# Kernel optimization log

Hardware: AMD Instinct MI355X
Metric: run time of the kernel (lower is better)

Reference implementation:

```python
import jax, jax.numpy as jnp
import numpy as np

B, T, H, L, FUT = 64, 256, 512, 4, 64


def setup_inputs() -> dict:
    key = jax.random.key(0)
    ks = jax.random.split(key, 8)
    s = 1.0 / np.sqrt(H)  # PyTorch LSTMCell/Linear default uniform init bound
    u = lambda k, shape: jax.random.uniform(k, shape, jnp.float32, -s, s)
    return {
        "iput": jax.random.normal(ks[0], (B, T), jnp.float32),
        "W_ih0": u(ks[1], (4 * H, 1)),        # layer 0 input->gates
        "W_ih": u(ks[2], (L - 1, 4 * H, H)),  # layers 1..L-1 input->gates
        "W_hh": u(ks[3], (L, 4 * H, H)),      # hidden->gates, all layers
        "b_ih": u(ks[4], (L, 4 * H)),
        "b_hh": u(ks[5], (L, 4 * H)),
        "W_lin": u(ks[6], (1, H)),            # readout Linear(H, 1)
        "b_lin": u(ks[7], (1,)),
        "future": FUT,
    }


def _cell(x, h, c, Wi, Wh, bi, bh):
    # PyTorch LSTMCell: gates ordered i, f, g, o
    g = x @ Wi.T + h @ Wh.T + bi + bh  # [B, 4H]
    i, f, gg, o = jnp.split(g, 4, axis=-1)
    c2 = jax.nn.sigmoid(f) * c + jax.nn.sigmoid(i) * jnp.tanh(gg)
    h2 = jax.nn.sigmoid(o) * jnp.tanh(c2)
    return h2, c2


def reference(iput, W_ih0, W_ih, W_hh, b_ih, b_hh, W_lin, b_lin, future):
    Lc = W_hh.shape[0]
    Bsz = iput.shape[0]
    Hd = W_hh.shape[-1]

    def layers(x, hs, cs):  # x: [B,1]; hs,cs: [L,B,H]
        for j in range(Lc):
            Wi = W_ih0 if j == 0 else W_ih[j - 1]
            inp = x if j == 0 else hs[j - 1]
            h2, c2 = _cell(inp, hs[j], cs[j], Wi, W_hh[j], b_ih[j], b_hh[j])
            hs = hs.at[j].set(h2)
            cs = cs.at[j].set(c2)
        return hs, cs

    hs0 = jnp.zeros((Lc, Bsz, Hd), iput.dtype)
    cs0 = jnp.zeros_like(hs0)

    def step_in(carry, x_t):  # x_t: [B]
        hs, cs = carry
        hs, cs = layers(x_t[:, None], hs, cs)
        out = hs[-1] @ W_lin.T + b_lin  # [B,1]
        return (hs, cs), out[:, 0]

    (hs, cs), outs = jax.lax.scan(step_in, (hs0, cs0), iput.T)  # outs: [T,B]

    def step_fut(carry, _):
        hs, cs, out = carry
        hs, cs = layers(out, hs, cs)
        out2 = hs[-1] @ W_lin.T + b_lin
        return (hs, cs, out2), out2[:, 0]

    last_out = outs[-1][:, None]  # feed last prediction back
    _, fouts = jax.lax.scan(step_fut, (hs, cs, last_out), None, length=future)

    return jnp.concatenate([outs, fouts], axis=0).T  # [B, T+future]
```

## Files before the change

### kernel.cpp

```cpp
#include <hip/hip_runtime.h>

#define Bsz 64
#define Tn 256
#define Hn 512
#define Ln 4
#define Gn 2048
#define TTn 320
#define NBLK 256
#define NTHR 512
#define HB (Hn * Bsz)
#define LHB (Ln * HB)
#define NPH_W (Tn + Ln - 1)

typedef float f32x4 __attribute__((ext_vector_type(4)));

#define OFF_WHH  0
#define OFF_WIH  (OFF_WHH + Ln * 8 * Hn)
#define OFF_PART (OFF_WIH + (Ln - 1) * 8 * Hn)
#define OFF_BS   (OFF_PART + 8 * 8 * Bsz)
#define OFF_W0   (OFF_BS + Ln * 8)
#define OFF_WLIN (OFF_W0 + 8)
#define OFF_RP   (OFF_WLIN + Hn)
#define OFF_XS   (OFF_RP + 8 * Bsz)
#define OFF_C    (OFF_XS + Bsz)
#define SMEM_FLOATS (OFF_C + Ln * 2 * Bsz)
#define SMEM_BYTES (SMEM_FLOATS * 4)

#define WS_BCOUNT   0
#define WS_ARRIVE   16
#define WS_MASTER   (16 + 16 * 32)
#define WS_BOOT     (WS_MASTER + 32)
#define WS_BOOTFLAG (WS_BOOT + 32)
#define WS_U32S     (WS_BOOTFLAG + 32)

__device__ float g_h[2 * LHB];
__device__ float g_hist[Tn * HB];
__device__ float g_p[Bsz * NBLK];
__device__ float g_xsg[Bsz];

__device__ __forceinline__ float sigm(float x) { return 1.0f / (1.0f + expf(-x)); }

__device__ __forceinline__ void fma4v(f32x4& a, const f32x4 h, const float w) {
    a.x = fmaf(h.x, w, a.x); a.y = fmaf(h.y, w, a.y);
    a.z = fmaf(h.z, w, a.z); a.w = fmaf(h.w, w, a.w);
}

#define GSTF(ptr, val) \
    asm volatile("global_store_dword %0, %1, off sc0 sc1" \
                 :: "v"(ptr), "v"(val) : "memory")
#define VMWAIT() asm volatile("s_waitcnt vmcnt(0)" ::: "memory")
#define L1INV() asm volatile("buffer_inv" ::: "memory")

__device__ __forceinline__ uint32_t rmw_add(uint32_t* p, uint32_t v) {
    return __hip_atomic_fetch_add(p, v, __ATOMIC_RELAXED, __HIP_MEMORY_SCOPE_AGENT);
}
__device__ __forceinline__ uint32_t ald(const uint32_t* p) {
    return __hip_atomic_load(p, __ATOMIC_RELAXED, __HIP_MEMORY_SCOPE_AGENT);
}
__device__ __forceinline__ uint32_t xcc_id() {
    uint32_t x;
    asm("s_getreg_b32 %0, hwreg(HW_REG_XCC_ID)" : "=s"(x));
    return x & 15u;
}

__device__ __forceinline__ void boot_bar(uint32_t* wsb, int tid) {
    VMWAIT();
    __syncthreads();
    if (tid == 0) {
        __builtin_amdgcn_fence(__ATOMIC_RELEASE, "agent");
        uint32_t old = rmw_add(wsb + WS_BOOT, 1u);
        if (old == NBLK - 1u) rmw_add(wsb + WS_BOOTFLAG, 1u);
        while (ald(wsb + WS_BOOTFLAG) < 1u) __builtin_amdgcn_s_sleep(2);
        __builtin_amdgcn_fence(__ATOMIC_ACQUIRE, "agent");
    }
    __syncthreads();
    asm volatile("" ::: "memory");
}

__device__ __forceinline__ void gbar(uint32_t* wsb, int tid, uint32_t x,
                                     uint32_t cnt_x, uint32_t& e) {
    ++e;
    VMWAIT();
    __syncthreads();
    if (tid == 0) {
        const uint32_t tgt = e * (uint32_t)NBLK;
        uint32_t old = rmw_add(wsb + WS_ARRIVE + x * 32, 1u);
        if (old == e * cnt_x - 1u) {
            __builtin_amdgcn_fence(__ATOMIC_ACQUIRE, "agent");
            VMWAIT();
            rmw_add(wsb + WS_MASTER, cnt_x);
            while (ald(wsb + WS_MASTER) < tgt) {}
        } else {
            while (ald(wsb + WS_MASTER) < tgt) {}
            L1INV();
            VMWAIT();
        }
    }
    __syncthreads();
    asm volatile("" ::: "memory");
}

__device__ __forceinline__ void gemm16(const float* __restrict__ w,
                                       const float* __restrict__ hbase,
                                       int k0, int b4, f32x4* acc) {
#pragma unroll
    for (int c = 0; c < 4; ++c) {
        const int k = k0 + c * 4;
        const float* hp = hbase + (size_t)k * Bsz + b4;
        const f32x4 h0 = *(const f32x4*)(hp);
        const f32x4 h1 = *(const f32x4*)(hp + Bsz);
        const f32x4 h2 = *(const f32x4*)(hp + 2 * Bsz);
        const f32x4 h3 = *(const f32x4*)(hp + 3 * Bsz);
#pragma unroll
        for (int r = 0; r < 8; ++r) {
            const f32x4 wv = *(const f32x4*)(w + r * Hn + k);
            fma4v(acc[r], h0, wv.x); fma4v(acc[r], h1, wv.y);
            fma4v(acc[r], h2, wv.z); fma4v(acc[r], h3, wv.w);
        }
    }
}

__global__ __launch_bounds__(NTHR, 1)
void lstm_seq(const float* __restrict__ iput,
              const float* __restrict__ Wih0,
              const float* __restrict__ Wih,
              const float* __restrict__ Whh,
              const float* __restrict__ bih,
              const float* __restrict__ bhh,
              const float* __restrict__ Wlin,
              const float* __restrict__ blin,
              float* __restrict__ out,
              uint32_t* __restrict__ wsb)
{
    extern __shared__ float sm[];
    const int bi  = blockIdx.x;
    const int tid = threadIdx.x;
    uint32_t e = 0;

    const uint32_t x = xcc_id();
    uint32_t cnt_x = 0;
    if (tid == 0) rmw_add(wsb + WS_BCOUNT + x, 1u);

    for (int i = tid; i < Ln * 8 * Hn; i += NTHR) {
        const int lyr = i >> 12, rem = i & 4095, r = rem >> 9, k = rem & 511;
        sm[OFF_WHH + i] = Whh[((size_t)(lyr * Gn + (r & 3) * Hn + bi * 2 + (r >> 2))) * Hn + k];
    }
    for (int i = tid; i < (Ln - 1) * 8 * Hn; i += NTHR) {
        const int lyr = i >> 12, rem = i & 4095, r = rem >> 9, k = rem & 511;
        sm[OFF_WIH + i] = Wih[((size_t)(lyr * Gn + (r & 3) * Hn + bi * 2 + (r >> 2))) * Hn + k];
    }
    if (tid < Ln * 8) {
        const int lyr = tid >> 3, r = tid & 7;
        const int gg = lyr * Gn + (r & 3) * Hn + bi * 2 + (r >> 2);
        sm[OFF_BS + tid] = bih[gg] + bhh[gg];
    }
    if (tid < 8) sm[OFF_W0 + tid] = Wih0[(tid & 3) * Hn + bi * 2 + (tid >> 2)];
    for (int i = tid; i < Hn; i += NTHR) sm[OFF_WLIN + i] = Wlin[i];
    for (int i = tid; i < Ln * 2 * Bsz; i += NTHR) sm[OFF_C + i] = 0.0f;

    for (int i = bi * NTHR + tid; i < 2 * LHB; i += NBLK * NTHR)
        GSTF(&g_h[i], 0.0f);

    const float blin0 = blin[0];
    boot_bar(wsb, tid);
    if (tid == 0) cnt_x = ald(wsb + WS_BCOUNT + x);

    {
        const int l   = tid >> 7;
        const int sub = tid & 127;
        const int bgw = sub & 15, b4w = bgw * 4;
        const int kgw = sub >> 4;
        const int k0w = kgw * 64;
        const int w2  = (tid >> 6) & 1;

        for (int s = 0; s < NPH_W; ++s) {
            const int pp = s & 1;
            float* cur        = g_h + pp * LHB;
            const float* prev = g_h + (pp ^ 1) * LHB;
            const int t = s - l;
            const bool act = ((unsigned)t < (unsigned)Tn);

            f32x4 acc[8];
#pragma unroll
            for (int r = 0; r < 8; ++r) acc[r] = (f32x4){0.f, 0.f, 0.f, 0.f};

            if (act) {
                {
                    const float* wh  = sm + OFF_WHH + l * 8 * Hn;
                    const float* hp0 = prev + (size_t)l * HB;
#pragma unroll 4
                    for (int c = 0; c < 16; ++c) {
                        const int k = k0w + (((c + (kgw & 3) * 4) & 15) << 2);
                        const float* hp = hp0 + (size_t)k * Bsz + b4w;
                        const f32x4 h0 = *(const f32x4*)(hp);
                        const f32x4 h1 = *(const f32x4*)(hp + Bsz);
                        const f32x4 h2 = *(const f32x4*)(hp + 2 * Bsz);
                        const f32x4 h3 = *(const f32x4*)(hp + 3 * Bsz);
#pragma unroll
                        for (int r = 0; r < 8; ++r) {
                            const f32x4 wv = *(const f32x4*)(wh + r * Hn + k);
                            fma4v(acc[r], h0, wv.x); fma4v(acc[r], h1, wv.y);
                            fma4v(acc[r], h2, wv.z); fma4v(acc[r], h3, wv.w);
                        }
                    }
                }
                if (l > 0) {
                    const float* wh  = sm + OFF_WIH + (l - 1) * 8 * Hn;
                    const float* hp0 = prev + (size_t)(l - 1) * HB;
#pragma unroll 4
                    for (int c = 0; c < 16; ++c) {
                        const int k = k0w + (((c + (kgw & 3) * 4) & 15) << 2);
                        const float* hp = hp0 + (size_t)k * Bsz + b4w;
                        const f32x4 h0 = *(const f32x4*)(hp);
                        const f32x4 h1 = *(const f32x4*)(hp + Bsz);
                        const f32x4 h2 = *(const f32x4*)(hp + 2 * Bsz);
                        const f32x4 h3 = *(const f32x4*)(hp + 3 * Bsz);
#pragma unroll
                        for (int r = 0; r < 8; ++r) {
                            const f32x4 wv = *(const f32x4*)(wh + r * Hn + k);
                            fma4v(acc[r], h0, wv.x); fma4v(acc[r], h1, wv.y);
                            fma4v(acc[r], h2, wv.z); fma4v(acc[r], h3, wv.w);
                        }
                    }
                }
            }

#pragma unroll
            for (int r = 0; r < 8; ++r) {
                f32x4 a = acc[r];
                a.x += __shfl_xor(a.x, 16); a.y += __shfl_xor(a.y, 16);
                a.z += __shfl_xor(a.z, 16); a.w += __shfl_xor(a.w, 16);
                a.x += __shfl_xor(a.x, 32); a.y += __shfl_xor(a.y, 32);
                a.z += __shfl_xor(a.z, 32); a.w += __shfl_xor(a.w, 32);
                acc[r] = a;
            }
            if ((tid & 48) == 0) {
#pragma unroll
                for (int r = 0; r < 8; ++r)
                    *(f32x4*)&sm[OFF_PART + ((l * 2 + w2) * 8 + r) * Bsz + b4w] = acc[r];
            }
            __syncthreads();

            {
                const int lb = tid >> 7, jl = (tid >> 6) & 1, b = tid & 63;
                const int tb = s - lb;
                if ((unsigned)tb < (unsigned)Tn) {
                    const int jg = bi * 2 + jl;
                    float gv[4];
#pragma unroll
                    for (int q = 0; q < 4; ++q) {
                        const int r = (jl << 2) | q;
                        gv[q] = sm[OFF_BS + lb * 8 + r]
                              + sm[OFF_PART + ((lb * 2 + 0) * 8 + r) * Bsz + b]
                              + sm[OFF_PART + ((lb * 2 + 1) * 8 + r) * Bsz + b];
                    }
                    if (lb == 0) {
                        const float xv = iput[b * Tn + s];
#pragma unroll
                        for (int q = 0; q < 4; ++q)
                            gv[q] = fmaf(xv, sm[OFF_W0 + ((jl << 2) | q)], gv[q]);
                    }
                    const float i_ = sigm(gv[0]);
                    const float f_ = sigm(gv[1]);
                    const float g_ = tanhf(gv[2]);
                    const float o_ = sigm(gv[3]);
                    float* cp = sm + OFF_C + (lb * 2 + jl) * Bsz + b;
                    const float c2 = fmaf(f_, *cp, i_ * g_);
                    *cp = c2;
                    const float h2 = o_ * tanhf(c2);
                    GSTF(&cur[((size_t)lb * Hn + jg) * Bsz + b], h2);
                    if (lb == 3)
                        GSTF(&g_hist[((size_t)tb * Hn + jg) * Bsz + b], h2);
                }
            }
            gbar(wsb, tid, x, cnt_x, e);
        }
    }

    {
        const int b = tid & 63, jq = tid >> 6;
        const float* hp = g_hist + ((size_t)bi * Hn + jq * 64) * Bsz + b;
        const float* wp = sm + OFF_WLIN + jq * 64;
        float r = 0.0f;
#pragma unroll 8
        for (int j = 0; j < 64; ++j) r = fmaf(hp[j * Bsz], wp[j], r);
        sm[OFF_RP + jq * Bsz + b] = r;
        if (tid < 256) {
            const int li = (tid >> 7) * 2 + 1;
            const int jl = (tid >> 6) & 1, bb = tid & 63;
            const size_t o = ((size_t)li * Hn + bi * 2 + jl) * Bsz + bb;
            const float v = g_h[o];
            GSTF(&g_h[LHB + o], v);
        }
        __syncthreads();
        if (tid < Bsz) {
            float xx = blin0;
#pragma unroll
            for (int q = 0; q < 8; ++q) xx += sm[OFF_RP + q * Bsz + tid];
            out[tid * TTn + bi] = xx;
            if (bi == 255) GSTF(&g_xsg[tid], xx);
        }
        gbar(wsb, tid, x, cnt_x, e);
    }

    {
        const int bg  = tid & 15, b4 = bg * 4;
        const int kg  = tid >> 4;
        const int k0  = kg * 16;
        const int wv_ = tid >> 6;

        for (int t = Tn; t < TTn; ++t) {
            const int ci = t & 1;
            float* hcur        = g_h + ci * LHB;
            const float* hprev = g_h + (ci ^ 1) * LHB;

            for (int lyr = 0; lyr < Ln; ++lyr) {
                if (lyr == 0 && tid < Bsz) {
                    float xx;
                    if (t == Tn) {
                        xx = g_xsg[tid];
                    } else {
                        const f32x4* pp2 = (const f32x4*)(g_p + tid * NBLK);
                        f32x4 s4 = {0.f, 0.f, 0.f, 0.f};
#pragma unroll 16
                        for (int q = 0; q < NBLK / 4; ++q) s4 += pp2[q];
                        xx = s4.x + s4.y + s4.z + s4.w + blin0;
                        if (bi == ((t - 1) & 255))
                            out[tid * TTn + (t - 1)] = xx;
                    }
                    sm[OFF_XS + tid] = xx;
                }

                f32x4 acc[8];
#pragma unroll
                for (int r = 0; r < 8; ++r) acc[r] = (f32x4){0.f, 0.f, 0.f, 0.f};

                if (lyr > 0)
                    gemm16(sm + OFF_WIH + (lyr - 1) * 8 * Hn,
                           hcur + (size_t)(lyr - 1) * HB, k0, b4, acc);
                gemm16(sm + OFF_WHH + lyr * 8 * Hn,
                       hprev + (size_t)lyr * HB, k0, b4, acc);

#pragma unroll
                for (int r = 0; r < 8; ++r) {
                    f32x4 a = acc[r];
                    a.x += __shfl_xor(a.x, 16); a.y += __shfl_xor(a.y, 16);
                    a.z += __shfl_xor(a.z, 16); a.w += __shfl_xor(a.w, 16);
                    a.x += __shfl_xor(a.x, 32); a.y += __shfl_xor(a.y, 32);
                    a.z += __shfl_xor(a.z, 32); a.w += __shfl_xor(a.w, 32);
                    acc[r] = a;
                }
                if ((tid & 48) == 0) {
#pragma unroll
                    for (int r = 0; r < 8; ++r)
                        *(f32x4*)&sm[OFF_PART + (wv_ * 8 + r) * Bsz + b4] = acc[r];
                }
                __syncthreads();

                float h2 = 0.0f;
                if (tid < 128) {
                    const int jl = tid >> 6, b = tid & 63;
                    const int jg = bi * 2 + jl;
                    float gv[4];
#pragma unroll
                    for (int q = 0; q < 4; ++q) {
                        const int r = (jl << 2) | q;
                        float v = sm[OFF_BS + lyr * 8 + r];
#pragma unroll
                        for (int p = 0; p < 8; ++p)
                            v += sm[OFF_PART + (p * 8 + r) * Bsz + b];
                        if (lyr == 0)
                            v = fmaf(sm[OFF_XS + b], sm[OFF_W0 + r], v);
                        gv[q] = v;
                    }
                    const float i_ = sigm(gv[0]);
                    const float f_ = sigm(gv[1]);
                    const float g_ = tanhf(gv[2]);
                    const float o_ = sigm(gv[3]);
                    float* cp = sm + OFF_C + (lyr * 2 + jl) * Bsz + b;
                    const float c2 = fmaf(f_, *cp, i_ * g_);
                    *cp = c2;
                    h2 = o_ * tanhf(c2);
                    GSTF(&hcur[((size_t)lyr * Hn + jg) * Bsz + b], h2);
                    if (lyr == 3 && jl == 1)
                        sm[OFF_RP + b] = h2 * sm[OFF_WLIN + jg];
                }
                if (lyr == 3) {
                    __syncthreads();
                    if (tid < Bsz) {
                        const float pv = fmaf(h2, sm[OFF_WLIN + bi * 2], sm[OFF_RP + tid]);
                        GSTF(&g_p[tid * NBLK + bi], pv);
                    }
                }

                gbar(wsb, tid, x, cnt_x, e);
            }
        }
    }

    if (bi == 0 && tid < Bsz) {
        const f32x4* pp2 = (const f32x4*)(g_p + tid * NBLK);
        f32x4 s4 = {0.f, 0.f, 0.f, 0.f};
#pragma unroll 16
        for (int q = 0; q < NBLK / 4; ++q) s4 += pp2[q];
        out[tid * TTn + (TTn - 1)] = s4.x + s4.y + s4.z + s4.w + blin0;
    }
}

extern "C" void kernel_launch(void* const* d_in, const int* in_sizes, int n_in,
                              void* d_out, int out_size, void* d_ws, size_t ws_size,
                              hipStream_t stream) {
    const float* iput = (const float*)d_in[0];
    const float* Wih0 = (const float*)d_in[1];
    const float* Wih  = (const float*)d_in[2];
    const float* Whh  = (const float*)d_in[3];
    const float* bih  = (const float*)d_in[4];
    const float* bhh  = (const float*)d_in[5];
    const float* Wlin = (const float*)d_in[6];
    const float* blin = (const float*)d_in[7];
    float* out = (float*)d_out;
    uint32_t* wsb = (uint32_t*)d_ws;

    (void)hipFuncSetAttribute((const void*)lstm_seq,
                              hipFuncAttributeMaxDynamicSharedMemorySize, SMEM_BYTES);

    (void)hipMemsetAsync(d_ws, 0, WS_U32S * sizeof(uint32_t), stream);

    void* args[] = {&iput, &Wih0, &Wih, &Whh, &bih, &bhh, &Wlin, &blin, &out, &wsb};
    hipLaunchCooperativeKernel((const void*)lstm_seq, dim3(NBLK), dim3(NTHR), args,
                               SMEM_BYTES, stream);
}
```

Measured before the change: 9.115 ms.

## Double threads per block and split gate GEMM rows across waves

Raises the block size from 512 to 1024 threads. Each wave now computes 2 gate rows over a quarter of K instead of 8 rows over a slice of K, which shrinks the per-thread accumulator set and the partial-sum reduction buffer. The wavefront pipeline, the readout partial sums and the autoregressive phase are all remapped to match. More resident waves could hide shared- and global-memory latency, but each wave now rereads the h vectors once per row pair rather than once per 8 rows, which raises total global/L2 load traffic.

```diff
diff --git a/kernel.cpp b/kernel.cpp
--- a/kernel.cpp
+++ b/kernel.cpp
@@ -7,7 +7,7 @@
 #define Gn 2048
 #define TTn 320
 #define NBLK 256
-#define NTHR 512
+#define NTHR 1024
 #define HB (Hn * Bsz)
 #define LHB (Ln * HB)
 #define NPH_W (Tn + Ln - 1)
@@ -17,11 +17,11 @@
 #define OFF_WHH  0
 #define OFF_WIH  (OFF_WHH + Ln * 8 * Hn)
 #define OFF_PART (OFF_WIH + (Ln - 1) * 8 * Hn)
-#define OFF_BS   (OFF_PART + 8 * 8 * Bsz)
+#define OFF_BS   (OFF_PART + 4 * 8 * Bsz)
 #define OFF_W0   (OFF_BS + Ln * 8)
 #define OFF_WLIN (OFF_W0 + 8)
 #define OFF_RP   (OFF_WLIN + Hn)
-#define OFF_XS   (OFF_RP + 8 * Bsz)
+#define OFF_XS   (OFF_RP + 16 * Bsz)
 #define OFF_C    (OFF_XS + Bsz)
 #define SMEM_FLOATS (OFF_C + Ln * 2 * Bsz)
 #define SMEM_BYTES (SMEM_FLOATS * 4)
@@ -100,24 +100,36 @@
     asm volatile("" ::: "memory");
 }
 
-__device__ __forceinline__ void gemm16(const float* __restrict__ w,
-                                       const float* __restrict__ hbase,
-                                       int k0, int b4, f32x4* acc) {
-#pragma unroll
-    for (int c = 0; c < 4; ++c) {
+template <int NITER>
+__device__ __forceinline__ void gemm_rows2(const float* __restrict__ wrow,
+                                           const float* __restrict__ hbase,
+                                           int k0, int b4, f32x4& a0, f32x4& a1) {
+#pragma unroll 4
+    for (int c = 0; c < NITER; ++c) {
         const int k = k0 + c * 4;
         const float* hp = hbase + (size_t)k * Bsz + b4;
         const f32x4 h0 = *(const f32x4*)(hp);
         const f32x4 h1 = *(const f32x4*)(hp + Bsz);
         const f32x4 h2 = *(const f32x4*)(hp + 2 * Bsz);
         const f32x4 h3 = *(const f32x4*)(hp + 3 * Bsz);
-#pragma unroll
-        for (int r = 0; r < 8; ++r) {
-            const f32x4 wv = *(const f32x4*)(w + r * Hn + k);
-            fma4v(acc[r], h0, wv.x); fma4v(acc[r], h1, wv.y);
-            fma4v(acc[r], h2, wv.z); fma4v(acc[r], h3, wv.w);
-        }
-    }
+        const f32x4 w0 = *(const f32x4*)(wrow + k);
+        const f32x4 w1 = *(const f32x4*)(wrow + Hn + k);
+        fma4v(a0, h0, w0.x); fma4v(a0, h1, w0.y);
+        fma4v(a0, h2, w0.z); fma4v(a0, h3, w0.w);
+        fma4v(a1, h0, w1.x); fma4v(a1, h1, w1.y);
+        fma4v(a1, h2, w1.z); fma4v(a1, h3, w1.w);
+    }
+}
+
+__device__ __forceinline__ void wave_reduce2(f32x4& a0, f32x4& a1) {
+    a0.x += __shfl_xor(a0.x, 16); a0.y += __shfl_xor(a0.y, 16);
+    a0.z += __shfl_xor(a0.z, 16); a0.w += __shfl_xor(a0.w, 16);
+    a1.x += __shfl_xor(a1.x, 16); a1.y += __shfl_xor(a1.y, 16);
+    a1.z += __shfl_xor(a1.z, 16); a1.w += __shfl_xor(a1.w, 16);
+    a0.x += __shfl_xor(a0.x, 32); a0.y += __shfl_xor(a0.y, 32);
+    a0.z += __shfl_xor(a0.z, 32); a0.w += __shfl_xor(a0.w, 32);
+    a1.x += __shfl_xor(a1.x, 32); a1.y += __shfl_xor(a1.y, 32);
+    a1.z += __shfl_xor(a1.z, 32); a1.w += __shfl_xor(a1.w, 32);
 }
 
 __global__ __launch_bounds__(NTHR, 1)
@@ -166,12 +178,13 @@
     if (tid == 0) cnt_x = ald(wsb + WS_BCOUNT + x);
 
     {
-        const int l   = tid >> 7;
-        const int sub = tid & 127;
+        const int l   = tid >> 8;
+        const int sub = tid & 255;
         const int bgw = sub & 15, b4w = bgw * 4;
-        const int kgw = sub >> 4;
-        const int k0w = kgw * 64;
-        const int w2  = (tid >> 6) & 1;
+        const int kq  = (sub >> 4) & 3;
+        const int w2  = sub >> 6;
+        const int k0w = kq * 128;
+        const int r0  = w2 * 2;
 
         for (int s = 0; s < NPH_W; ++s) {
             const int pp = s & 1;
@@ -180,68 +193,22 @@
             const int t = s - l;
             const bool act = ((unsigned)t < (unsigned)Tn);
 
-            f32x4 acc[8];
-#pragma unroll
-            for (int r = 0; r < 8; ++r) acc[r] = (f32x4){0.f, 0.f, 0.f, 0.f};
-
+            f32x4 a0 = {0.f, 0.f, 0.f, 0.f}, a1 = {0.f, 0.f, 0.f, 0.f};
             if (act) {
-                {
-                    const float* wh  = sm + OFF_WHH + l * 8 * Hn;
-                    const float* hp0 = prev + (size_t)l * HB;
-#pragma unroll 4
-                    for (int c = 0; c < 16; ++c) {
-                        const int k = k0w + (((c + (kgw & 3) * 4) & 15) << 2);
-                        const float* hp = hp0 + (size_t)k * Bsz + b4w;
-                        const f32x4 h0 = *(const f32x4*)(hp);
-                        const f32x4 h1 = *(const f32x4*)(hp + Bsz);
-                        const f32x4 h2 = *(const f32x4*)(hp + 2 * Bsz);
-                        const f32x4 h3 = *(const f32x4*)(hp + 3 * Bsz);
-#pragma unroll
-                        for (int r = 0; r < 8; ++r) {
-                            const f32x4 wv = *(const f32x4*)(wh + r * Hn + k);
-                            fma4v(acc[r], h0, wv.x); fma4v(acc[r], h1, wv.y);
-                            fma4v(acc[r], h2, wv.z); fma4v(acc[r], h3, wv.w);
-                        }
-                    }
-                }
-                if (l > 0) {
-                    const float* wh  = sm + OFF_WIH + (l - 1) * 8 * Hn;
-                    const float* hp0 = prev + (size_t)(l - 1) * HB;
-#pragma unroll 4
-                    for (int c = 0; c < 16; ++c) {
-                        const int k = k0w + (((c + (kgw & 3) * 4) & 15) << 2);
-                        const float* hp = hp0 + (size_t)k * Bsz + b4w;
-                        const f32x4 h0 = *(const f32x4*)(hp);
-                        const f32x4 h1 = *(const f32x4*)(hp + Bsz);
-                        const f32x4 h2 = *(const f32x4*)(hp + 2 * Bsz);
-                        const f32x4 h3 = *(const f32x4*)(hp + 3 * Bsz);
-#pragma unroll
-                        for (int r = 0; r < 8; ++r) {
-                            const f32x4 wv = *(const f32x4*)(wh + r * Hn + k);
-                            fma4v(acc[r], h0, wv.x); fma4v(acc[r], h1, wv.y);
-                            fma4v(acc[r], h2, wv.z); fma4v(acc[r], h3, wv.w);
-                        }
-                    }
-                }
+                gemm_rows2<32>(sm + OFF_WHH + (l * 8 + r0) * Hn,
+                               prev + (size_t)l * HB, k0w, b4w, a0, a1);
+                if (l > 0)
+                    gemm_rows2<32>(sm + OFF_WIH + ((l - 1) * 8 + r0) * Hn,
+                                   prev + (size_t)(l - 1) * HB, k0w, b4w, a0, a1);
             }
-
-#pragma unroll
-            for (int r = 0; r < 8; ++r) {
-                f32x4 a = acc[r];
-                a.x += __shfl_xor(a.x, 16); a.y += __shfl_xor(a.y, 16);
-                a.z += __shfl_xor(a.z, 16); a.w += __shfl_xor(a.w, 16);
-                a.x += __shfl_xor(a.x, 32); a.y += __shfl_xor(a.y, 32);
-                a.z += __shfl_xor(a.z, 32); a.w += __shfl_xor(a.w, 32);
-                acc[r] = a;
-            }
+            wave_reduce2(a0, a1);
             if ((tid & 48) == 0) {
-#pragma unroll
-                for (int r = 0; r < 8; ++r)
-                    *(f32x4*)&sm[OFF_PART + ((l * 2 + w2) * 8 + r) * Bsz + b4w] = acc[r];
+                *(f32x4*)&sm[OFF_PART + ((l * 8 + r0 + 0) * Bsz) + b4w] = a0;
+                *(f32x4*)&sm[OFF_PART + ((l * 8 + r0 + 1) * Bsz) + b4w] = a1;
             }
             __syncthreads();
 
-            {
+            if (tid < 512) {
                 const int lb = tid >> 7, jl = (tid >> 6) & 1, b = tid & 63;
                 const int tb = s - lb;
                 if ((unsigned)tb < (unsigned)Tn) {
@@ -251,8 +218,7 @@
                     for (int q = 0; q < 4; ++q) {
                         const int r = (jl << 2) | q;
                         gv[q] = sm[OFF_BS + lb * 8 + r]
-                              + sm[OFF_PART + ((lb * 2 + 0) * 8 + r) * Bsz + b]
-                              + sm[OFF_PART + ((lb * 2 + 1) * 8 + r) * Bsz + b];
+                              + sm[OFF_PART + (lb * 8 + r) * Bsz + b];
                     }
                     if (lb == 0) {
                         const float xv = iput[b * Tn + s];
@@ -279,11 +245,11 @@
 
     {
         const int b = tid & 63, jq = tid >> 6;
-        const float* hp = g_hist + ((size_t)bi * Hn + jq * 64) * Bsz + b;
-        const float* wp = sm + OFF_WLIN + jq * 64;
+        const float* hp = g_hist + ((size_t)bi * Hn + jq * 32) * Bsz + b;
+        const float* wp = sm + OFF_WLIN + jq * 32;
         float r = 0.0f;
 #pragma unroll 8
-        for (int j = 0; j < 64; ++j) r = fmaf(hp[j * Bsz], wp[j], r);
+        for (int j = 0; j < 32; ++j) r = fmaf(hp[j * Bsz], wp[j], r);
         sm[OFF_RP + jq * Bsz + b] = r;
         if (tid < 256) {
             const int li = (tid >> 7) * 2 + 1;
@@ -296,7 +262,7 @@
         if (tid < Bsz) {
             float xx = blin0;
 #pragma unroll
-            for (int q = 0; q < 8; ++q) xx += sm[OFF_RP + q * Bsz + tid];
+            for (int q = 0; q < 16; ++q) xx += sm[OFF_RP + q * Bsz + tid];
             out[tid * TTn + bi] = xx;
             if (bi == 255) GSTF(&g_xsg[tid], xx);
         }
@@ -305,9 +271,11 @@
 
     {
         const int bg  = tid & 15, b4 = bg * 4;
-        const int kg  = tid >> 4;
-        const int k0  = kg * 16;
-        const int wv_ = tid >> 6;
+        const int kq2 = (tid >> 4) & 3;
+        const int w   = tid >> 6;
+        const int r0  = (w & 3) * 2;
+        const int kh  = w >> 2;
+        const int k0  = kh * 128 + kq2 * 32;
 
         for (int t = Tn; t < TTn; ++t) {
             const int ci = t & 1;
@@ -331,29 +299,17 @@
                     sm[OFF_XS + tid] = xx;
                 }
 
-                f32x4 acc[8];
-#pragma unroll
-                for (int r = 0; r < 8; ++r) acc[r] = (f32x4){0.f, 0.f, 0.f, 0.f};
-
+                f32x4 a0 = {0.f, 0.f, 0.f, 0.f}, a1 = {0.f, 0.f, 0.f, 0.f};
                 if (lyr > 0)
-                    gemm16(sm + OFF_WIH + (lyr - 1) * 8 * Hn,
-                           hcur + (size_t)(lyr - 1) * HB, k0, b4, acc);
-                gemm16(sm + OFF_WHH + lyr * 8 * Hn,
-                       hprev + (size_t)lyr * HB, k0, b4, acc);
-
-#pragma unroll
-                for (int r = 0; r < 8; ++r) {
-                    f32x4 a = acc[r];
-                    a.x += __shfl_xor(a.x, 16); a.y += __shfl_xor(a.y, 16);
-                    a.z += __shfl_xor(a.z, 16); a.w += __shfl_xor(a.w, 16);
-                    a.x += __shfl_xor(a.x, 32); a.y += __shfl_xor(a.y, 32);
-                    a.z += __shfl_xor(a.z, 32); a.w += __shfl_xor(a.w, 32);
-                    acc[r] = a;
-                }
+                    gemm_rows2<8>(sm + OFF_WIH + ((lyr - 1) * 8 + r0) * Hn,
+                                  hcur + (size_t)(lyr - 1) * HB, k0, b4, a0, a1);
+                gemm_rows2<8>(sm + OFF_WHH + (lyr * 8 + r0) * Hn,
+                              hprev + (size_t)lyr * HB, k0, b4, a0, a1);
+
+                wave_reduce2(a0, a1);
                 if ((tid & 48) == 0) {
-#pragma unroll
-                    for (int r = 0; r < 8; ++r)
-                        *(f32x4*)&sm[OFF_PART + (wv_ * 8 + r) * Bsz + b4] = acc[r];
+                    *(f32x4*)&sm[OFF_PART + ((kh * 8 + r0 + 0) * Bsz) + b4] = a0;
+                    *(f32x4*)&sm[OFF_PART + ((kh * 8 + r0 + 1) * Bsz) + b4] = a1;
                 }
                 __syncthreads();
 
@@ -367,7 +323,7 @@
                         const int r = (jl << 2) | q;
                         float v = sm[OFF_BS + lyr * 8 + r];
 #pragma unroll
-                        for (int p = 0; p < 8; ++p)
+                        for (int p = 0; p < 4; ++p)
                             v += sm[OFF_PART + (p * 8 + r) * Bsz + b];
                         if (lyr == 0)
                             v = fmaf(sm[OFF_XS + b], sm[OFF_W0 + r], v);
```

Result: slower. 10.38 ms (+13.9%).
